# Kernel tuning notes

Measured on AMD Instinct MI355X. Metric: run time of the kernel, lower is better.

Reference implementation:

```python
import jax, jax.numpy as jnp
import numpy as np

B, D, H, W, C = 2, 8, 64, 64, 128
NH = 8
WS = (2, 8, 8)
SS = (1, 4, 4)
HEAD_DIM = C // NH
SCALE = HEAD_DIM ** -0.5
MLP_HIDDEN = 4 * C


def _window_partition(x, ws):
    # x: (B, D, H, W, C) -> (B*nW, ws0*ws1*ws2, C)
    b, d, h, w, c = x.shape
    x = x.reshape(b, d // ws[0], ws[0], h // ws[1], ws[1], w // ws[2], ws[2], c)
    return x.transpose(0, 1, 3, 5, 2, 4, 6, 7).reshape(-1, ws[0] * ws[1] * ws[2], c)


def _window_reverse(win, ws, b, d, h, w):
    x = win.reshape(b, d // ws[0], h // ws[1], w // ws[2], ws[0], ws[1], ws[2], -1)
    return x.transpose(0, 1, 4, 2, 5, 3, 6, 7).reshape(b, d, h, w, -1)


def _rel_pos_index(ws):
    coords = np.stack(np.meshgrid(np.arange(ws[0]), np.arange(ws[1]), np.arange(ws[2]), indexing='ij'))
    cf = coords.reshape(3, -1)                       # (3, N)
    rel = (cf[:, :, None] - cf[:, None, :]).transpose(1, 2, 0)  # (N, N, 3)
    rel[:, :, 0] += ws[0] - 1
    rel[:, :, 1] += ws[1] - 1
    rel[:, :, 2] += ws[2] - 1
    rel[:, :, 0] *= (2 * ws[1] - 1) * (2 * ws[2] - 1)
    rel[:, :, 1] *= 2 * ws[2] - 1
    return rel.sum(-1)                               # (N, N)


def _attn_mask(d, h, w, ws, ss):
    img = np.zeros((1, d, h, w, 1), np.float32)
    cnt = 0
    for sd in (slice(-ws[0]), slice(-ws[0], -ss[0]), slice(-ss[0], None)):
        for sh in (slice(-ws[1]), slice(-ws[1], -ss[1]), slice(-ss[1], None)):
            for sw in (slice(-ws[2]), slice(-ws[2], -ss[2]), slice(-ss[2], None)):
                img[:, sd, sh, sw, :] = cnt
                cnt += 1
    mw = _window_partition(img, ws)[..., 0]          # (nW, N)
    am = mw[:, None, :] - mw[:, :, None]             # (nW, N, N)
    return np.where(am != 0, -100.0, 0.0).astype(np.float32)


def _ln(x, g, b):
    m = x.mean(-1, keepdims=True)
    v = ((x - m) ** 2).mean(-1, keepdims=True)
    return (x - m) / jnp.sqrt(v + 1e-5) * g + b


def setup_inputs() -> dict:
    key = jax.random.key(0)
    ks = jax.random.split(key, 8)
    n_bias = (2 * WS[0] - 1) * (2 * WS[1] - 1) * (2 * WS[2] - 1)
    return {
        'x': jax.random.normal(ks[0], (B, D, H, W, C), jnp.float32),
        'qkv_w': jax.random.normal(ks[1], (3 * C, C), jnp.float32) * 0.02,
        'qkv_b': jnp.zeros((3 * C,), jnp.float32),
        'proj_w': jax.random.normal(ks[2], (C, C), jnp.float32) * 0.02,
        'proj_b': jnp.zeros((C,), jnp.float32),
        'rpb': jax.random.normal(ks[3], (n_bias, NH), jnp.float32) * 0.02,
        'ln1_g': jnp.ones((C,), jnp.float32),
        'ln1_b': jnp.zeros((C,), jnp.float32),
        'ln2_g': jnp.ones((C,), jnp.float32),
        'ln2_b': jnp.zeros((C,), jnp.float32),
        'fc1_w': jax.random.normal(ks[4], (MLP_HIDDEN, C), jnp.float32) * 0.02,
        'fc1_b': jnp.zeros((MLP_HIDDEN,), jnp.float32),
        'fc2_w': jax.random.normal(ks[5], (C, MLP_HIDDEN), jnp.float32) * 0.02,
        'fc2_b': jnp.zeros((C,), jnp.float32),
    }


def reference(x, qkv_w, qkv_b, proj_w, proj_b, rpb, ln1_g, ln1_b, ln2_g, ln2_b, fc1_w, fc1_b, fc2_w, fc2_b):
    shortcut = x
    xn = _ln(x, ln1_g, ln1_b)
    # cyclic shift (SW-MSA)
    xs = jnp.roll(xn, (-SS[0], -SS[1], -SS[2]), axis=(1, 2, 3))
    win = _window_partition(xs, WS)                  # (Bw, N, C)
    Bw, N, _ = win.shape
    qkv = (win @ qkv_w.T + qkv_b).reshape(Bw, N, 3, NH, HEAD_DIM).transpose(2, 0, 3, 1, 4)
    q, k, v = qkv[0] * SCALE, qkv[1], qkv[2]         # (Bw, NH, N, d)
    attn = jnp.einsum('bhnd,bhmd->bhnm', q, k)       # (Bw, NH, N, N)
    rpi = _rel_pos_index(WS)
    bias = rpb[rpi.reshape(-1)].reshape(N, N, NH).transpose(2, 0, 1)  # (NH, N, N)
    attn = attn + bias[None]
    mask = jnp.asarray(_attn_mask(D, H, W, WS, SS))  # (nW, N, N)
    nW = mask.shape[0]
    attn = attn.reshape(B, nW, NH, N, N) + mask[None, :, None]
    attn = jax.nn.softmax(attn, axis=-1).reshape(Bw, NH, N, N)
    out = jnp.einsum('bhnm,bhmd->bhnd', attn, v).transpose(0, 2, 1, 3).reshape(Bw, N, C)
    out = out @ proj_w.T + proj_b
    xr = _window_reverse(out, WS, B, D, H, W)
    xr = jnp.roll(xr, SS, axis=(1, 2, 3))
    x1 = shortcut + xr
    # MLP block
    y = _ln(x1, ln2_g, ln2_b)
    y = jax.nn.gelu(y @ fc1_w.T + fc1_b, approximate=False)
    y = y @ fc2_w.T + fc2_b
    return x1 + y
```

## Files before the change

kernel.cpp:

```cpp
#include <hip/hip_runtime.h>
#include <math.h>

typedef short s16x8 __attribute__((ext_vector_type(8)));
typedef short s16x4 __attribute__((ext_vector_type(4)));
typedef float f32x4 __attribute__((ext_vector_type(4)));

#define MFMA(a, b, c)    __builtin_amdgcn_mfma_f32_16x16x32_bf16(a, b, c, 0, 0, 0)
#define MFMA16(a, b, c)  __builtin_amdgcn_mfma_f32_16x16x16bf16_1k(a, b, c, 0, 0, 0)

__device__ __forceinline__ float b2f(ushort u) {
    union { unsigned int i; float f; } v; v.i = ((unsigned int)u) << 16; return v.f;
}
__device__ __forceinline__ ushort f2b(float f) {
    union { float f; unsigned int i; } v; v.f = f;
    unsigned int r = v.i + 0x7fffu + ((v.i >> 16) & 1u);
    return (ushort)(r >> 16);
}
__device__ __forceinline__ float gelu_tanh(float v) {
    float u = 0.7978845608f * (v + 0.044715f * v * v * v);
    float e = __expf(-2.f * fabsf(u));
    float t = (1.f - e) / (1.f + e);
    t = (u < 0.f) ? -t : t;
    return 0.5f * v * (1.f + t);
}

__global__ __launch_bounds__(256) void k0_prep(
    const float* __restrict__ qkv_w, const float* __restrict__ proj_w,
    const float* __restrict__ fc1_w, const float* __restrict__ fc2_w,
    const float* __restrict__ rpb, ushort* __restrict__ wq,
    ushort* __restrict__ wp, ushort* __restrict__ wf, ushort* __restrict__ bm)
{
    int bid = blockIdx.x, tid = threadIdx.x;
    if (bid < 192) { int idx = bid * 256 + tid; wq[idx] = f2b(qkv_w[idx]); return; }
    if (bid < 256) { int idx = (bid - 192) * 256 + tid; wp[idx] = f2b(proj_w[idx]); return; }
    if (bid < 768) {
        int idx = (bid - 256) * 256 + tid;
        wf[idx] = f2b(idx < 65536 ? fc1_w[idx] : fc2_w[idx - 65536]);
        return;
    }
    int bi = bid - 768;
    int cls = bi >> 3, head = bi & 7;
    int ed = (cls >> 2) & 1, eh = (cls >> 1) & 1, ew = cls & 1;
    int j = tid & 127;
    int tdj = j >> 6, thj = (j >> 3) & 7, twj = j & 7;
    int regj = (ed ? (tdj + 1) : 0) * 9
             + (eh ? ((thj < 4) ? 1 : 2) : 0) * 3
             + (ew ? ((twj < 4) ? 1 : 2) : 0);
    ushort* bmp = bm + (long)bi * 16384;
    for (int ii = 0; ii < 64; ++ii) {
        int i = (tid >> 7) * 64 + ii;
        int tdi = i >> 6, thi = (i >> 3) & 7, twi = i & 7;
        int regi = (ed ? (tdi + 1) : 0) * 9
                 + (eh ? ((thi < 4) ? 1 : 2) : 0) * 3
                 + (ew ? ((twi < 4) ? 1 : 2) : 0);
        int rpi = (tdi - tdj + 1) * 225 + (thi - thj + 7) * 15 + (twi - twj + 7);
        float v = rpb[rpi * 8 + head] + ((regi != regj) ? -100.f : 0.f);
        bmp[i * 128 + j] = f2b(v);
    }
}

__global__ __launch_bounds__(256) void k2_qkv(
    const float* __restrict__ x, const float* __restrict__ g,
    const float* __restrict__ be, const ushort* __restrict__ wq,
    const float* __restrict__ qkv_b, ushort* __restrict__ qkv)
{
    __shared__ __align__(16) ushort As[128][136];
    int tid = threadIdx.x;
    int m0 = blockIdx.x * 128;
    {
        int row = tid >> 1, half = tid & 1;
        int tk = m0 + row;
        int wi = tk >> 7, t = tk & 127;
        int b = wi >> 8, wd = (wi >> 6) & 3, wh = (wi >> 3) & 7, ww = wi & 7;
        int td = t >> 6, th = (t >> 3) & 7, tw = t & 7;
        int d = (wd * 2 + td + 1) & 7;
        int h = (wh * 8 + th + 4) & 63;
        int w = (ww * 8 + tw + 4) & 63;
        long src = (((long)((b * 8 + d) * 64 + h)) * 64 + w) * 128 + half * 64;
        float vals[64];
        float s = 0.f, q = 0.f;
        #pragma unroll
        for (int i = 0; i < 16; ++i) {
            float4 u = *(const float4*)&x[src + i * 4];
            vals[i * 4 + 0] = u.x; vals[i * 4 + 1] = u.y;
            vals[i * 4 + 2] = u.z; vals[i * 4 + 3] = u.w;
            s += u.x + u.y + u.z + u.w;
            q += u.x * u.x + u.y * u.y + u.z * u.z + u.w * u.w;
        }
        s += __shfl_xor(s, 1);
        q += __shfl_xor(q, 1);
        float mean = s * (1.f / 128.f);
        float rstd = rsqrtf(q * (1.f / 128.f) - mean * mean + 1e-5f);
        #pragma unroll
        for (int i = 0; i < 8; ++i) {
            ushort pk[8];
            #pragma unroll
            for (int jj = 0; jj < 8; ++jj) {
                int c = half * 64 + i * 8 + jj;
                pk[jj] = f2b((vals[i * 8 + jj] - mean) * rstd * g[c] + be[c]);
            }
            *(uint4*)&As[row][half * 64 + i * 8] = *(uint4*)pk;
        }
    }
    __syncthreads();
    int wv = tid >> 6, lane = tid & 63, li = lane & 15, quad = lane >> 4;
    int wm = wv >> 1, wn = wv & 1;
    long wibase = (long)(m0 >> 7) * 49152;
    for (int nb = 0; nb < 3; ++nb) {
        f32x4 acc[4][4] = {};
        for (int s = 0; s < 4; ++s) {
            s16x8 a[4], bw[4];
            #pragma unroll
            for (int mi = 0; mi < 4; ++mi)
                a[mi] = *(const s16x8*)&As[wm * 64 + mi * 16 + li][s * 32 + quad * 8];
            #pragma unroll
            for (int ni = 0; ni < 4; ++ni)
                bw[ni] = *(const s16x8*)&wq[(long)(nb * 128 + wn * 64 + ni * 16 + li) * 128
                                            + s * 32 + quad * 8];
            #pragma unroll
            for (int mi = 0; mi < 4; ++mi)
                #pragma unroll
                for (int ni = 0; ni < 4; ++ni)
                    acc[mi][ni] = MFMA(a[mi], bw[ni], acc[mi][ni]);
        }
        #pragma unroll
        for (int mi = 0; mi < 4; ++mi)
            #pragma unroll
            for (int ni = 0; ni < 4; ++ni) {
                int gcol = nb * 128 + wn * 64 + ni * 16 + li;
                int mat = gcol >> 7, hd = (gcol >> 4) & 7;
                float bias = qkv_b[gcol];
                float scale = (mat == 0) ? 0.25f : 1.f;
                long base2 = wibase + mat * 16384 + hd * 2048 + li;
                #pragma unroll
                for (int r = 0; r < 4; ++r) {
                    int trow = wm * 64 + mi * 16 + quad * 4 + r;
                    qkv[base2 + trow * 16] = f2b((acc[mi][ni][r] + bias) * scale);
                }
            }
    }
}

__global__ __launch_bounds__(64) void k3_attn(
    ushort* __restrict__ qkv, const ushort* __restrict__ bm)
{
    __shared__ __align__(16) ushort vt[16][136];
    __shared__ __align__(16) ushort ks[128][24];
    int b = blockIdx.x;
    int h = b & 7, wi = b >> 3;
    int wd = (wi >> 6) & 3, wh = (wi >> 3) & 7, ww = wi & 7;
    int cls = ((wd == 3) << 2) | ((wh == 7) << 1) | (ww == 7);
    int lane = threadIdx.x;
    int li = lane & 15, quad = lane >> 4;
    long hb = (long)wi * 49152 + h * 2048;
    #pragma unroll
    for (int t2 = 0; t2 < 2; ++t2) {
        int tok = t2 * 64 + lane;
        const ushort* vp = &qkv[hb + 32768 + tok * 16];
        uint4 v0 = *(const uint4*)vp;
        uint4 v1 = *(const uint4*)(vp + 8);
        const ushort* p0 = (const ushort*)&v0;
        const ushort* p1 = (const ushort*)&v1;
        #pragma unroll
        for (int j = 0; j < 8; ++j) { vt[j][tok] = p0[j]; vt[8 + j][tok] = p1[j]; }
        const ushort* kp = &qkv[hb + 16384 + tok * 16];
        *(uint4*)&ks[tok][0] = *(const uint4*)kp;
        *(uint4*)&ks[tok][8] = *(const uint4*)(kp + 8);
    }
    __syncthreads();
    long bmb = (long)(cls * 8 + h) * 16384;
    for (int qq = 0; qq < 4; ++qq) {
        int row0 = qq * 32;
        s16x4 qf0 = *(const s16x4*)&qkv[hb + (row0 + li) * 16 + quad * 4];
        s16x4 qf1 = *(const s16x4*)&qkv[hb + (row0 + 16 + li) * 16 + quad * 4];
        float ps0 = 0.f, ps1 = 0.f;
        uint pa0[8][2], pa1[8][2];
        #pragma unroll
        for (int mi = 0; mi < 8; ++mi) {
            s16x4 kf = *(const s16x4*)&ks[mi * 16 + li][quad * 4];
            f32x4 z = {0.f, 0.f, 0.f, 0.f};
            f32x4 s0 = MFMA16(kf, qf0, z);
            f32x4 s1 = MFMA16(kf, qf1, z);
            s16x4 b0 = *(const s16x4*)&bm[bmb + (row0 + li) * 128 + mi * 16 + quad * 4];
            s16x4 b1 = *(const s16x4*)&bm[bmb + (row0 + 16 + li) * 128 + mi * 16 + quad * 4];
            float e0 = __expf(s0[0] + b2f((ushort)b0[0]));
            float e1 = __expf(s0[1] + b2f((ushort)b0[1]));
            float e2 = __expf(s0[2] + b2f((ushort)b0[2]));
            float e3 = __expf(s0[3] + b2f((ushort)b0[3]));
            ps0 += (e0 + e1) + (e2 + e3);
            pa0[mi][0] = (uint)f2b(e0) | ((uint)f2b(e1) << 16);
            pa0[mi][1] = (uint)f2b(e2) | ((uint)f2b(e3) << 16);
            float f0 = __expf(s1[0] + b2f((ushort)b1[0]));
            float f1 = __expf(s1[1] + b2f((ushort)b1[1]));
            float f2 = __expf(s1[2] + b2f((ushort)b1[2]));
            float f3 = __expf(s1[3] + b2f((ushort)b1[3]));
            ps1 += (f0 + f1) + (f2 + f3);
            pa1[mi][0] = (uint)f2b(f0) | ((uint)f2b(f1) << 16);
            pa1[mi][1] = (uint)f2b(f2) | ((uint)f2b(f3) << 16);
        }
        ps0 += __shfl_xor(ps0, 16); ps0 += __shfl_xor(ps0, 32);
        ps1 += __shfl_xor(ps1, 16); ps1 += __shfl_xor(ps1, 32);
        float inv0 = 1.f / ps0, inv1 = 1.f / ps1;
        f32x4 pc0 = {0.f, 0.f, 0.f, 0.f}, pc1 = {0.f, 0.f, 0.f, 0.f};
        #pragma unroll
        for (int mi = 0; mi < 8; ++mi) {
            s16x4 vf = *(const s16x4*)&vt[li][mi * 16 + quad * 4];
            union { uint2 u; s16x4 v; } a0, a1;
            a0.u.x = pa0[mi][0]; a0.u.y = pa0[mi][1];
            a1.u.x = pa1[mi][0]; a1.u.y = pa1[mi][1];
            pc0 = MFMA16(a0.v, vf, pc0);
            pc1 = MFMA16(a1.v, vf, pc1);
        }
        #pragma unroll
        for (int r = 0; r < 4; ++r) {
            float oi0 = __shfl(inv0, quad * 4 + r);
            float oi1 = __shfl(inv1, quad * 4 + r);
            int i0 = row0 + quad * 4 + r;
            int i1 = row0 + 16 + quad * 4 + r;
            qkv[hb + (long)i0 * 16 + li] = f2b(pc0[r] * oi0);
            qkv[hb + (long)i1 * 16 + li] = f2b(pc1[r] * oi1);
        }
    }
}

__global__ __launch_bounds__(256) void k45(
    const ushort* __restrict__ ao, const ushort* __restrict__ wp,
    const float* __restrict__ proj_b, const float* __restrict__ x,
    const float* __restrict__ g2, const float* __restrict__ be2,
    const ushort* __restrict__ wf1, const float* __restrict__ fc1_b,
    const ushort* __restrict__ wf2, const float* __restrict__ fc2_b,
    float* __restrict__ out)
{
    __shared__ __align__(16) ushort As[64][132];
    __shared__ __align__(16) ushort x1t[64][132];
    __shared__ __align__(16) ushort hs[64][132];
    __shared__ float redS[4][64];
    __shared__ float redQ[4][64];
    int tid = threadIdx.x;
    int b = blockIdx.x;
    int wi = b >> 1, half64 = b & 1;
    int wd = (wi >> 6) & 3, wh = (wi >> 3) & 7, ww = wi & 7;
    int bb = wi >> 8;
    long aob = (long)wi * 49152;
    int tok0 = half64 * 64;
    #pragma unroll
    for (int i = 0; i < 4; ++i) {
        int slot = tid + i * 256;
        int row = slot & 63, hsl = slot >> 6;
        *(uint4*)&As[row][hsl * 8] =
            *(const uint4*)&ao[aob + (hsl >> 1) * 2048 + (long)(tok0 + row) * 16 + (hsl & 1) * 8];
    }
    __syncthreads();
    int wv = tid >> 6, lane = tid & 63, li = lane & 15, quad = lane >> 4;
    int wm = wv >> 1, wn = wv & 1;
    f32x4 acc[2][4] = {};
    for (int s = 0; s < 4; ++s) {
        s16x8 a[2], bw[4];
        #pragma unroll
        for (int mi = 0; mi < 2; ++mi)
            a[mi] = *(const s16x8*)&As[wm * 32 + mi * 16 + li][s * 32 + quad * 8];
        #pragma unroll
        for (int ni = 0; ni < 4; ++ni)
            bw[ni] = *(const s16x8*)&wp[(long)(wn * 64 + ni * 16 + li) * 128 + s * 32 + quad * 8];
        #pragma unroll
        for (int mi = 0; mi < 2; ++mi)
            #pragma unroll
            for (int ni = 0; ni < 4; ++ni)
                acc[mi][ni] = MFMA(a[mi], bw[ni], acc[mi][ni]);
    }
    #pragma unroll
    for (int mi = 0; mi < 2; ++mi) {
        #pragma unroll
        for (int r = 0; r < 4; ++r) {
            int lrow = wm * 32 + mi * 16 + quad * 4 + r;
            int t = half64 * 64 + lrow;
            int td = t >> 6, th = (t >> 3) & 7, tw = t & 7;
            int d = (wd * 2 + td + 1) & 7, h = (wh * 8 + th + 4) & 63, w = (ww * 8 + tw + 4) & 63;
            long di = (((long)((bb * 8 + d) * 64 + h)) * 64 + w) * 128;
            #pragma unroll
            for (int ni = 0; ni < 4; ++ni) {
                int col = wn * 64 + ni * 16 + li;
                x1t[lrow][col] = f2b(acc[mi][ni][r] + proj_b[col] + x[di + col]);
            }
        }
    }
    __syncthreads();
    {
        int token = tid & 63, part = tid >> 6;
        float vals[32];
        float s = 0.f, q = 0.f;
        #pragma unroll
        for (int i = 0; i < 4; ++i) {
            uint4 u = *(const uint4*)&x1t[token][part * 32 + i * 8];
            const ushort* p = (const ushort*)&u;
            #pragma unroll
            for (int j = 0; j < 8; ++j) { float f = b2f(p[j]); vals[i * 8 + j] = f; s += f; q += f * f; }
        }
        redS[part][token] = s; redQ[part][token] = q;
        __syncthreads();
        float st = 0.f, qt = 0.f;
        #pragma unroll
        for (int p2 = 0; p2 < 4; ++p2) { st += redS[p2][token]; qt += redQ[p2][token]; }
        float mean = st * (1.f / 128.f);
        float rstd = rsqrtf(qt * (1.f / 128.f) - mean * mean + 1e-5f);
        #pragma unroll
        for (int i = 0; i < 4; ++i) {
            ushort packed[8];
            #pragma unroll
            for (int j = 0; j < 8; ++j) {
                int c = part * 32 + i * 8 + j;
                packed[j] = f2b((vals[i * 8 + j] - mean) * rstd * g2[c] + be2[c]);
            }
            *(uint4*)&As[token][part * 32 + i * 8] = *(uint4*)packed;
        }
    }
    __syncthreads();
    f32x4 yacc[2][4] = {};
    for (int hc = 0; hc < 4; ++hc) {
        f32x4 hacc[2][4] = {};
        #pragma unroll
        for (int kk = 0; kk < 4; ++kk) {
            s16x8 a[2], bw[4];
            #pragma unroll
            for (int mi = 0; mi < 2; ++mi)
                a[mi] = *(const s16x8*)&As[wm * 32 + mi * 16 + li][kk * 32 + quad * 8];
            #pragma unroll
            for (int ni = 0; ni < 4; ++ni)
                bw[ni] = *(const s16x8*)&wf1[(long)(hc * 128 + wn * 64 + ni * 16 + li) * 128
                                             + kk * 32 + quad * 8];
            #pragma unroll
            for (int mi = 0; mi < 2; ++mi)
                #pragma unroll
                for (int ni = 0; ni < 4; ++ni)
                    hacc[mi][ni] = MFMA(a[mi], bw[ni], hacc[mi][ni]);
        }
        #pragma unroll
        for (int mi = 0; mi < 2; ++mi)
            #pragma unroll
            for (int ni = 0; ni < 4; ++ni) {
                int col = wn * 64 + ni * 16 + li;
                float bbv = fc1_b[hc * 128 + col];
                #pragma unroll
                for (int r = 0; r < 4; ++r) {
                    int row = wm * 32 + mi * 16 + quad * 4 + r;
                    hs[row][col] = f2b(gelu_tanh(hacc[mi][ni][r] + bbv));
                }
            }
        __syncthreads();
        #pragma unroll
        for (int kk = 0; kk < 4; ++kk) {
            s16x8 a[2], bw[4];
            #pragma unroll
            for (int mi = 0; mi < 2; ++mi)
                a[mi] = *(const s16x8*)&hs[wm * 32 + mi * 16 + li][kk * 32 + quad * 8];
            #pragma unroll
            for (int ni = 0; ni < 4; ++ni)
                bw[ni] = *(const s16x8*)&wf2[(long)(wn * 64 + ni * 16 + li) * 512
                                             + hc * 128 + kk * 32 + quad * 8];
            #pragma unroll
            for (int mi = 0; mi < 2; ++mi)
                #pragma unroll
                for (int ni = 0; ni < 4; ++ni)
                    yacc[mi][ni] = MFMA(a[mi], bw[ni], yacc[mi][ni]);
        }
        __syncthreads();
    }
    #pragma unroll
    for (int mi = 0; mi < 2; ++mi) {
        #pragma unroll
        for (int r = 0; r < 4; ++r) {
            int lrow = wm * 32 + mi * 16 + quad * 4 + r;
            int t = half64 * 64 + lrow;
            int td = t >> 6, th = (t >> 3) & 7, tw = t & 7;
            int d = (wd * 2 + td + 1) & 7, h = (wh * 8 + th + 4) & 63, w = (ww * 8 + tw + 4) & 63;
            long di = (((long)((bb * 8 + d) * 64 + h)) * 64 + w) * 128;
            #pragma unroll
            for (int ni = 0; ni < 4; ++ni) {
                int col = wn * 64 + ni * 16 + li;
                out[di + col] = b2f(x1t[lrow][col]) + yacc[mi][ni][r] + fc2_b[col];
            }
        }
    }
}

extern "C" void kernel_launch(void* const* d_in, const int* in_sizes, int n_in,
                              void* d_out, int out_size, void* d_ws, size_t ws_size,
                              hipStream_t stream)
{
    (void)in_sizes; (void)n_in; (void)out_size; (void)ws_size;
    const float* x      = (const float*)d_in[0];
    const float* qkv_w  = (const float*)d_in[1];
    const float* qkv_b  = (const float*)d_in[2];
    const float* proj_w = (const float*)d_in[3];
    const float* proj_b = (const float*)d_in[4];
    const float* rpb    = (const float*)d_in[5];
    const float* ln1_g  = (const float*)d_in[6];
    const float* ln1_b  = (const float*)d_in[7];
    const float* ln2_g  = (const float*)d_in[8];
    const float* ln2_b  = (const float*)d_in[9];
    const float* fc1_w  = (const float*)d_in[10];
    const float* fc1_b  = (const float*)d_in[11];
    const float* fc2_w  = (const float*)d_in[12];
    const float* fc2_b  = (const float*)d_in[13];
    float* out = (float*)d_out;

    ushort* qkvb = (ushort*)d_ws;
    ushort* wq   = (ushort*)((char*)d_ws + 50331648);
    ushort* wp   = wq + 49152;
    ushort* wf   = wp + 16384;
    ushort* bm   = wf + 131072;

    hipLaunchKernelGGL(k0_prep, dim3(832), dim3(256), 0, stream,
                       qkv_w, proj_w, fc1_w, fc2_w, rpb, wq, wp, wf, bm);
    hipLaunchKernelGGL(k2_qkv, dim3(512), dim3(256), 0, stream,
                       x, ln1_g, ln1_b, wq, qkv_b, qkvb);
    hipLaunchKernelGGL(k3_attn, dim3(4096), dim3(64), 0, stream, qkvb, bm);
    hipLaunchKernelGGL(k45, dim3(1024), dim3(256), 0, stream,
                       qkvb, wp, proj_b, x, ln2_g, ln2_b,
                       wf, fc1_b, wf + 65536, fc2_b, out);
}
```

Before: 283.0 us.

## Fuse QKV projection and window attention into one kernel via shared memory

Merges the QKV GEMM kernel and the attention kernel so each block computes Q, K and V for a whole window into LDS and then runs attention for all 8 heads, two per wave. This removes the global round-trip of the full QKV tensor and one kernel launch, and the attention output buffer shrinks to one third of its former size. In exchange, LDS use per block rises to about 100KB and the attention work gets only 4 waves per window instead of 64-thread blocks per head, which may reduce occupancy and latency hiding.

```diff
diff --git a/kernel.cpp b/kernel.cpp
--- a/kernel.cpp
+++ b/kernel.cpp
@@ -59,20 +59,23 @@
     }
 }
 
-__global__ __launch_bounds__(256) void k2_qkv(
+__global__ __launch_bounds__(256) void k23(
     const float* __restrict__ x, const float* __restrict__ g,
     const float* __restrict__ be, const ushort* __restrict__ wq,
-    const float* __restrict__ qkv_b, ushort* __restrict__ qkv)
+    const float* __restrict__ qkv_b, const ushort* __restrict__ bm,
+    ushort* __restrict__ obuf)
 {
     __shared__ __align__(16) ushort As[128][136];
+    __shared__ __align__(16) ushort qb[128][132];
+    __shared__ __align__(16) ushort kb[128][132];
     int tid = threadIdx.x;
-    int m0 = blockIdx.x * 128;
+    int wi = blockIdx.x;
+    int wd = (wi >> 6) & 3, wh = (wi >> 3) & 7, ww = wi & 7;
+    int cls = ((wd == 3) << 2) | ((wh == 7) << 1) | (ww == 7);
     {
         int row = tid >> 1, half = tid & 1;
-        int tk = m0 + row;
-        int wi = tk >> 7, t = tk & 127;
-        int b = wi >> 8, wd = (wi >> 6) & 3, wh = (wi >> 3) & 7, ww = wi & 7;
-        int td = t >> 6, th = (t >> 3) & 7, tw = t & 7;
+        int b = wi >> 8;
+        int td = row >> 6, th = (row >> 3) & 7, tw = row & 7;
         int d = (wd * 2 + td + 1) & 7;
         int h = (wh * 8 + th + 4) & 63;
         int w = (ww * 8 + tw + 4) & 63;
@@ -105,7 +108,6 @@
     __syncthreads();
     int wv = tid >> 6, lane = tid & 63, li = lane & 15, quad = lane >> 4;
     int wm = wv >> 1, wn = wv & 1;
-    long wibase = (long)(m0 >> 7) * 49152;
     for (int nb = 0; nb < 3; ++nb) {
         f32x4 acc[4][4] = {};
         for (int s = 0; s < 4; ++s) {
@@ -123,102 +125,86 @@
                 for (int ni = 0; ni < 4; ++ni)
                     acc[mi][ni] = MFMA(a[mi], bw[ni], acc[mi][ni]);
         }
+        if (nb == 2) __syncthreads();
         #pragma unroll
         for (int mi = 0; mi < 4; ++mi)
             #pragma unroll
             for (int ni = 0; ni < 4; ++ni) {
                 int gcol = nb * 128 + wn * 64 + ni * 16 + li;
-                int mat = gcol >> 7, hd = (gcol >> 4) & 7;
                 float bias = qkv_b[gcol];
-                float scale = (mat == 0) ? 0.25f : 1.f;
-                long base2 = wibase + mat * 16384 + hd * 2048 + li;
+                float scale = (nb == 0) ? 0.25f : 1.f;
                 #pragma unroll
                 for (int r = 0; r < 4; ++r) {
                     int trow = wm * 64 + mi * 16 + quad * 4 + r;
-                    qkv[base2 + trow * 16] = f2b((acc[mi][ni][r] + bias) * scale);
+                    ushort val = f2b((acc[mi][ni][r] + bias) * scale);
+                    if (nb == 0) {
+                        qb[trow][gcol] = val;
+                    } else if (nb == 1) {
+                        kb[trow][gcol - 128] = val;
+                    } else {
+                        int c2 = gcol - 256, hh = c2 >> 4, dd = c2 & 15;
+                        ((ushort*)As)[hh * 2176 + dd * 136 + trow] = val;
+                    }
                 }
             }
     }
-}
-
-__global__ __launch_bounds__(64) void k3_attn(
-    ushort* __restrict__ qkv, const ushort* __restrict__ bm)
-{
-    __shared__ __align__(16) ushort vt[16][136];
-    __shared__ __align__(16) ushort ks[128][24];
-    int b = blockIdx.x;
-    int h = b & 7, wi = b >> 3;
-    int wd = (wi >> 6) & 3, wh = (wi >> 3) & 7, ww = wi & 7;
-    int cls = ((wd == 3) << 2) | ((wh == 7) << 1) | (ww == 7);
-    int lane = threadIdx.x;
-    int li = lane & 15, quad = lane >> 4;
-    long hb = (long)wi * 49152 + h * 2048;
-    #pragma unroll
-    for (int t2 = 0; t2 < 2; ++t2) {
-        int tok = t2 * 64 + lane;
-        const ushort* vp = &qkv[hb + 32768 + tok * 16];
-        uint4 v0 = *(const uint4*)vp;
-        uint4 v1 = *(const uint4*)(vp + 8);
-        const ushort* p0 = (const ushort*)&v0;
-        const ushort* p1 = (const ushort*)&v1;
-        #pragma unroll
-        for (int j = 0; j < 8; ++j) { vt[j][tok] = p0[j]; vt[8 + j][tok] = p1[j]; }
-        const ushort* kp = &qkv[hb + 16384 + tok * 16];
-        *(uint4*)&ks[tok][0] = *(const uint4*)kp;
-        *(uint4*)&ks[tok][8] = *(const uint4*)(kp + 8);
-    }
     __syncthreads();
-    long bmb = (long)(cls * 8 + h) * 16384;
-    for (int qq = 0; qq < 4; ++qq) {
-        int row0 = qq * 32;
-        s16x4 qf0 = *(const s16x4*)&qkv[hb + (row0 + li) * 16 + quad * 4];
-        s16x4 qf1 = *(const s16x4*)&qkv[hb + (row0 + 16 + li) * 16 + quad * 4];
-        float ps0 = 0.f, ps1 = 0.f;
-        uint pa0[8][2], pa1[8][2];
-        #pragma unroll
-        for (int mi = 0; mi < 8; ++mi) {
-            s16x4 kf = *(const s16x4*)&ks[mi * 16 + li][quad * 4];
-            f32x4 z = {0.f, 0.f, 0.f, 0.f};
-            f32x4 s0 = MFMA16(kf, qf0, z);
-            f32x4 s1 = MFMA16(kf, qf1, z);
-            s16x4 b0 = *(const s16x4*)&bm[bmb + (row0 + li) * 128 + mi * 16 + quad * 4];
-            s16x4 b1 = *(const s16x4*)&bm[bmb + (row0 + 16 + li) * 128 + mi * 16 + quad * 4];
-            float e0 = __expf(s0[0] + b2f((ushort)b0[0]));
-            float e1 = __expf(s0[1] + b2f((ushort)b0[1]));
-            float e2 = __expf(s0[2] + b2f((ushort)b0[2]));
-            float e3 = __expf(s0[3] + b2f((ushort)b0[3]));
-            ps0 += (e0 + e1) + (e2 + e3);
-            pa0[mi][0] = (uint)f2b(e0) | ((uint)f2b(e1) << 16);
-            pa0[mi][1] = (uint)f2b(e2) | ((uint)f2b(e3) << 16);
-            float f0 = __expf(s1[0] + b2f((ushort)b1[0]));
-            float f1 = __expf(s1[1] + b2f((ushort)b1[1]));
-            float f2 = __expf(s1[2] + b2f((ushort)b1[2]));
-            float f3 = __expf(s1[3] + b2f((ushort)b1[3]));
-            ps1 += (f0 + f1) + (f2 + f3);
-            pa1[mi][0] = (uint)f2b(f0) | ((uint)f2b(f1) << 16);
-            pa1[mi][1] = (uint)f2b(f2) | ((uint)f2b(f3) << 16);
-        }
-        ps0 += __shfl_xor(ps0, 16); ps0 += __shfl_xor(ps0, 32);
-        ps1 += __shfl_xor(ps1, 16); ps1 += __shfl_xor(ps1, 32);
-        float inv0 = 1.f / ps0, inv1 = 1.f / ps1;
-        f32x4 pc0 = {0.f, 0.f, 0.f, 0.f}, pc1 = {0.f, 0.f, 0.f, 0.f};
-        #pragma unroll
-        for (int mi = 0; mi < 8; ++mi) {
-            s16x4 vf = *(const s16x4*)&vt[li][mi * 16 + quad * 4];
-            union { uint2 u; s16x4 v; } a0, a1;
-            a0.u.x = pa0[mi][0]; a0.u.y = pa0[mi][1];
-            a1.u.x = pa1[mi][0]; a1.u.y = pa1[mi][1];
-            pc0 = MFMA16(a0.v, vf, pc0);
-            pc1 = MFMA16(a1.v, vf, pc1);
-        }
-        #pragma unroll
-        for (int r = 0; r < 4; ++r) {
-            float oi0 = __shfl(inv0, quad * 4 + r);
-            float oi1 = __shfl(inv1, quad * 4 + r);
-            int i0 = row0 + quad * 4 + r;
-            int i1 = row0 + 16 + quad * 4 + r;
-            qkv[hb + (long)i0 * 16 + li] = f2b(pc0[r] * oi0);
-            qkv[hb + (long)i1 * 16 + li] = f2b(pc1[r] * oi1);
+    const ushort* vtp = (const ushort*)As;
+    for (int hh2 = 0; hh2 < 2; ++hh2) {
+        int h = wv * 2 + hh2;
+        long bmb = (long)(cls * 8 + h) * 16384;
+        long ob = (long)wi * 16384 + h * 2048;
+        for (int qq = 0; qq < 4; ++qq) {
+            int row0 = qq * 32;
+            s16x4 qf0 = *(const s16x4*)&qb[row0 + li][h * 16 + quad * 4];
+            s16x4 qf1 = *(const s16x4*)&qb[row0 + 16 + li][h * 16 + quad * 4];
+            float ps0 = 0.f, ps1 = 0.f;
+            uint pa0[8][2], pa1[8][2];
+            #pragma unroll
+            for (int mi = 0; mi < 8; ++mi) {
+                s16x4 kf = *(const s16x4*)&kb[mi * 16 + li][h * 16 + quad * 4];
+                f32x4 z = {0.f, 0.f, 0.f, 0.f};
+                f32x4 s0 = MFMA16(kf, qf0, z);
+                f32x4 s1 = MFMA16(kf, qf1, z);
+                s16x4 b0 = *(const s16x4*)&bm[bmb + (row0 + li) * 128 + mi * 16 + quad * 4];
+                s16x4 b1 = *(const s16x4*)&bm[bmb + (row0 + 16 + li) * 128 + mi * 16 + quad * 4];
+                float e0 = __expf(s0[0] + b2f((ushort)b0[0]));
+                float e1 = __expf(s0[1] + b2f((ushort)b0[1]));
+                float e2 = __expf(s0[2] + b2f((ushort)b0[2]));
+                float e3 = __expf(s0[3] + b2f((ushort)b0[3]));
+                ps0 += (e0 + e1) + (e2 + e3);
+                pa0[mi][0] = (uint)f2b(e0) | ((uint)f2b(e1) << 16);
+                pa0[mi][1] = (uint)f2b(e2) | ((uint)f2b(e3) << 16);
+                float f0 = __expf(s1[0] + b2f((ushort)b1[0]));
+                float f1 = __expf(s1[1] + b2f((ushort)b1[1]));
+                float f2 = __expf(s1[2] + b2f((ushort)b1[2]));
+                float f3 = __expf(s1[3] + b2f((ushort)b1[3]));
+                ps1 += (f0 + f1) + (f2 + f3);
+                pa1[mi][0] = (uint)f2b(f0) | ((uint)f2b(f1) << 16);
+                pa1[mi][1] = (uint)f2b(f2) | ((uint)f2b(f3) << 16);
+            }
+            ps0 += __shfl_xor(ps0, 16); ps0 += __shfl_xor(ps0, 32);
+            ps1 += __shfl_xor(ps1, 16); ps1 += __shfl_xor(ps1, 32);
+            float inv0 = 1.f / ps0, inv1 = 1.f / ps1;
+            f32x4 pc0 = {0.f, 0.f, 0.f, 0.f}, pc1 = {0.f, 0.f, 0.f, 0.f};
+            #pragma unroll
+            for (int mi = 0; mi < 8; ++mi) {
+                s16x4 vf = *(const s16x4*)&vtp[h * 2176 + li * 136 + mi * 16 + quad * 4];
+                union { uint2 u; s16x4 v; } a0, a1;
+                a0.u.x = pa0[mi][0]; a0.u.y = pa0[mi][1];
+                a1.u.x = pa1[mi][0]; a1.u.y = pa1[mi][1];
+                pc0 = MFMA16(a0.v, vf, pc0);
+                pc1 = MFMA16(a1.v, vf, pc1);
+            }
+            #pragma unroll
+            for (int r = 0; r < 4; ++r) {
+                float oi0 = __shfl(inv0, quad * 4 + r);
+                float oi1 = __shfl(inv1, quad * 4 + r);
+                int i0 = row0 + quad * 4 + r;
+                int i1 = row0 + 16 + quad * 4 + r;
+                obuf[ob + (long)i0 * 16 + li] = f2b(pc0[r] * oi0);
+                obuf[ob + (long)i1 * 16 + li] = f2b(pc1[r] * oi1);
+            }
         }
     }
 }
@@ -241,7 +227,7 @@
     int wi = b >> 1, half64 = b & 1;
     int wd = (wi >> 6) & 3, wh = (wi >> 3) & 7, ww = wi & 7;
     int bb = wi >> 8;
-    long aob = (long)wi * 49152;
+    long aob = (long)wi * 16384;
     int tok0 = half64 * 64;
     #pragma unroll
     for (int i = 0; i < 4; ++i) {
@@ -404,7 +390,7 @@
     const float* fc2_b  = (const float*)d_in[13];
     float* out = (float*)d_out;
 
-    ushort* qkvb = (ushort*)d_ws;
+    ushort* obuf = (ushort*)d_ws;
     ushort* wq   = (ushort*)((char*)d_ws + 50331648);
     ushort* wp   = wq + 49152;
     ushort* wf   = wp + 16384;
@@ -412,10 +398,9 @@
 
     hipLaunchKernelGGL(k0_prep, dim3(832), dim3(256), 0, stream,
                        qkv_w, proj_w, fc1_w, fc2_w, rpb, wq, wp, wf, bm);
-    hipLaunchKernelGGL(k2_qkv, dim3(512), dim3(256), 0, stream,
-                       x, ln1_g, ln1_b, wq, qkv_b, qkvb);
-    hipLaunchKernelGGL(k3_attn, dim3(4096), dim3(64), 0, stream, qkvb, bm);
+    hipLaunchKernelGGL(k23, dim3(512), dim3(256), 0, stream,
+                       x, ln1_g, ln1_b, wq, qkv_b, bm, obuf);
     hipLaunchKernelGGL(k45, dim3(1024), dim3(256), 0, stream,
-                       qkvb, wp, proj_b, x, ln2_g, ln2_b,
+                       obuf, wp, proj_b, x, ln2_g, ln2_b,
                        wf, fc1_b, wf + 65536, fc2_b, out);
 }
```

New measurement: 269.6 us. 4.7% less time.
